# Kernel optimization log

Hardware: AMD Instinct MI355X
Metric: run time of the kernel (lower is better)

## Reference

```python
import jax, jax.numpy as jnp
import numpy as np


def _segmented_exclusive_cumsum(vals, seg_start_flags):
    """Exclusive cumsum of vals that resets at segment starts (flags True)."""
    def combine(a, b):
        va, fa = a
        vb, fb = b
        return (jnp.where(fb, vb, va + vb), fa | fb)
    inclusive, _ = jax.lax.associative_scan(combine, (vals, seg_start_flags))
    return inclusive - vals


def setup_inputs() -> dict:
    key = jax.random.key(0)
    k1, k2 = jax.random.split(key)
    n_rays = 65536
    samples_per_ray = 128  # average; ragged via sorted random ray ids
    n_pts = n_rays * samples_per_ray  # 8_388_608 sample points
    density = jax.random.normal(k1, (n_pts,), dtype=jnp.float32)
    ray_id = jnp.sort(jax.random.randint(k2, (n_pts,), 0, n_rays)).astype(jnp.int32)
    shift = jnp.float32(-3.0)      # self.act_shift
    interval = jnp.float32(0.5)    # stepsize * voxel_size_ratio
    return {"density": density, "shift": shift, "interval": interval,
            "ray_id": ray_id, "n_rays": n_rays}


def reference(density, shift, interval, ray_id, n_rays):
    # Raw2Alpha: alpha = 1 - exp(-softplus(density + shift) * interval)
    # log(1 - alpha) = -interval * softplus(density + shift)  (stable, no log of tiny)
    log_one_minus_alpha = -interval * jax.nn.softplus(density + shift)
    alpha = 1.0 - jnp.exp(log_one_minus_alpha)

    # Alphas2Weights: per-ray exclusive cumprod of (1 - alpha) in log space.
    # ray_id is sorted; segment starts where the ray id changes.
    seg_start = jnp.concatenate(
        [jnp.ones((1,), dtype=bool), ray_id[1:] != ray_id[:-1]])
    log_T = _segmented_exclusive_cumsum(log_one_minus_alpha, seg_start)
    T = jnp.exp(log_T)                      # transmittance before each sample
    weights = alpha * T                     # [n_pts]

    # alphainv_last[r] = prod over ray r of (1 - alpha) = residual transmittance
    log_total = jax.ops.segment_sum(log_one_minus_alpha, ray_id,
                                    num_segments=n_rays)
    alphainv_last = jnp.exp(log_total)      # [n_rays]; empty rays -> exp(0)=1
    return weights, alphainv_last
```

## Files before the change

### kernel.cpp

```cpp
#include <hip/hip_runtime.h>
#include <math.h>


#define LOG2E 1.4426950408889634f
#define EPT   8
#define BPTS  (256 * EPT)
#define NXCD  8

typedef float vf4 __attribute__((ext_vector_type(4)));

__device__ __forceinline__ float exp2f_(float x) { return __builtin_amdgcn_exp2f(x); }
__device__ __forceinline__ float log2f_(float x) { return __builtin_amdgcn_logf(x); }
__device__ __forceinline__ float rsqf_(float x)  { return __builtin_amdgcn_rsqf(x); }

__device__ __forceinline__ float oma(float d, float sh2, float negc, bool fast) {
    const float y = fmaf(d, LOG2E, sh2);
    if (fast) return rsqf_(1.0f + exp2f_(y));
    const float sp = fmaxf(y, 0.f) + log2f_(1.f + exp2f_(-fabsf(y)));
    return exp2f_(negc * sp);
}

template <int CTRL, int RM>
__device__ __forceinline__ void seg_step(float& V, int& F) {
    const int vs_i = __builtin_amdgcn_update_dpp(
        0x3f800000, __builtin_bit_cast(int, V), CTRL, RM, 0xF, false);
    const int fs = __builtin_amdgcn_update_dpp(0, F, CTRL, RM, 0xF, false);
    const float vs = __builtin_bit_cast(float, vs_i);
    V = F ? V : vs * V;
    F = F | fs;
}

__device__ __forceinline__ float wave_prod_bcast(float x) {
#define STEPP(CTRL, RM)                                                        \
    { int t_ = __builtin_amdgcn_update_dpp(0x3f800000,                         \
          __builtin_bit_cast(int, x), CTRL, RM, 0xF, false);                   \
      x *= __builtin_bit_cast(float, t_); }
    STEPP(0x111, 0xF) STEPP(0x112, 0xF) STEPP(0x114, 0xF)
    STEPP(0x118, 0xF) STEPP(0x142, 0xA) STEPP(0x143, 0xC)
#undef STEPP
    return __builtin_bit_cast(float,
        __builtin_amdgcn_readlane(__builtin_bit_cast(int, x), 63));
}

__device__ __forceinline__ int wave_imax_bcast(int x) {
#define STEPM(CTRL, RM)                                                        \
    { int t_ = __builtin_amdgcn_update_dpp((int)0x80000000, x, CTRL, RM,       \
                                           0xF, false);                        \
      x = (x > t_) ? x : t_; }
    STEPM(0x111, 0xF) STEPM(0x112, 0xF) STEPM(0x114, 0xF)
    STEPM(0x118, 0xF) STEPM(0x142, 0xA) STEPM(0x143, 0xC)
#undef STEPM
    return __builtin_amdgcn_readlane(x, 63);
}

__global__ void __launch_bounds__(256)
fused_alpha_weights(const float* __restrict__ density,
                    const int*   __restrict__ ray_id,
                    const float* __restrict__ shift_p,
                    const float* __restrict__ interval_p,
                    float* __restrict__ weights,
                    float* __restrict__ alphainv,
                    int n_pts, int n_rays) {
    __shared__ float s_wv[4];
    __shared__ int   s_wf[4];
    __shared__ float s_red[4];
    __shared__ int   s_redi[4];

    const int t    = threadIdx.x;
    const int lane = t & 63;
    const int wid  = t >> 6;

    const int nwg  = gridDim.x;
    const int orig = blockIdx.x;
    const int qq   = nwg / NXCD, rr = nwg % NXCD;
    const int xcd  = orig % NXCD;
    const int blk  = (xcd < rr ? xcd * (qq + 1) : rr * (qq + 1) + (xcd - rr) * qq)
                   + orig / NXCD;

    const int base = blk * BPTS;
    const int idx0 = base + t * EPT;

    const float shift = shift_p[0];
    const float c     = interval_p[0];
    const float sh2   = shift * LOG2E;
    const float negc  = -c;
    const bool  fast  = (c == 0.5f);

    int r[EPT + 1]; float d[EPT]; bool v[EPT];
    if (idx0 + EPT <= n_pts) {
        const int4   ri0 = *reinterpret_cast<const int4*>(ray_id + idx0);
        const int4   ri1 = *reinterpret_cast<const int4*>(ray_id + idx0 + 4);
        const float4 de0 = *reinterpret_cast<const float4*>(density + idx0);
        const float4 de1 = *reinterpret_cast<const float4*>(density + idx0 + 4);
        r[0] = ri0.x; r[1] = ri0.y; r[2] = ri0.z; r[3] = ri0.w;
        r[4] = ri1.x; r[5] = ri1.y; r[6] = ri1.z; r[7] = ri1.w;
        d[0] = de0.x; d[1] = de0.y; d[2] = de0.z; d[3] = de0.w;
        d[4] = de1.x; d[5] = de1.y; d[6] = de1.z; d[7] = de1.w;
        #pragma unroll
        for (int k = 0; k < EPT; ++k) v[k] = true;
    } else {
        #pragma unroll
        for (int k = 0; k < EPT; ++k) {
            const int i = idx0 + k;
            v[k] = (i < n_pts);
            r[k] = v[k] ? ray_id[i] : n_rays;
            d[k] = v[k] ? density[i] : 0.0f;
        }
    }
    r[EPT] = (idx0 + EPT < n_pts) ? ray_id[idx0 + EPT] : n_rays;
    const int rprev = (idx0 == 0) ? -1
                    : ((idx0 <= n_pts) ? ray_id[idx0 - 1] : n_rays);

    int w_id = 0; float w_den = 0.0f; int rfirst = 0;
    if (base > 0) {
        const int wi = base - 256 + t;
        w_id   = ray_id[wi];
        w_den  = density[wi];
        rfirst = ray_id[base];
    }

    float a[EPT]; int f[EPT];
    #pragma unroll
    for (int k = 0; k < EPT; ++k) {
        const float av = oma(d[k], sh2, negc, fast);
        a[k] = v[k] ? av : 1.0f;
        f[k] = (k == 0) ? (r[0] != rprev) : (r[k] != r[k - 1]);
    }

    float V = a[0];  int F = f[0];
    #pragma unroll
    for (int k = 1; k < EPT; ++k) {
        V = f[k] ? a[k] : V * a[k];
        F |= f[k];
    }

    float Vi = V;  int Fi = F;
    seg_step<0x111, 0xF>(Vi, Fi);
    seg_step<0x112, 0xF>(Vi, Fi);
    seg_step<0x114, 0xF>(Vi, Fi);
    seg_step<0x118, 0xF>(Vi, Fi);
    seg_step<0x142, 0xA>(Vi, Fi);
    seg_step<0x143, 0xC>(Vi, Fi);

    if (lane == 63) { s_wv[wid] = Vi; s_wf[wid] = Fi; }
    if (base > 0) {
        const int cand = (w_id != rfirst) ? t : -1;
        const int wm = wave_imax_bcast(cand);
        if (lane == 0) s_redi[wid] = wm;
    }
    __syncthreads();

    float carry0 = 1.0f;
    if (base > 0) {
        int m = s_redi[0];
        m = (s_redi[1] > m) ? s_redi[1] : m;
        m = (s_redi[2] > m) ? s_redi[2] : m;
        m = (s_redi[3] > m) ? s_redi[3] : m;
        float aa = oma(w_den, sh2, negc, fast);
        if (m >= 0 && t <= m) aa = 1.0f;
        const float wp = wave_prod_bcast(aa);
        if (lane == 0) s_red[wid] = wp;
        __syncthreads();
        carry0 = s_red[0] * s_red[1] * s_red[2] * s_red[3];

        if (m < 0) {
            int lo = base - 256;
            int s0 = -1;
            while (s0 < 0) {
                const int wstart = lo - 256;
                const int i = wstart + t;
                const int vv = (i >= 0) ? ray_id[i] : -1;
                const int c2 = (vv != rfirst) ? t : -1;
                const int wm2 = wave_imax_bcast(c2);
                if (lane == 0) s_redi[wid] = wm2;
                __syncthreads();
                int m2 = s_redi[0];
                m2 = (s_redi[1] > m2) ? s_redi[1] : m2;
                m2 = (s_redi[2] > m2) ? s_redi[2] : m2;
                m2 = (s_redi[3] > m2) ? s_redi[3] : m2;
                __syncthreads();
                if (m2 >= 0) s0 = wstart + m2 + 1; else lo = wstart;
            }
            for (int off = s0; off < base - 256; off += 256) {
                const int i = off + t;
                const float aa2 = (i < base - 256)
                                ? oma(density[i], sh2, negc, fast) : 1.0f;
                const float wp2 = wave_prod_bcast(aa2);
                if (lane == 0) s_red[wid] = wp2;
                __syncthreads();
                carry0 *= s_red[0] * s_red[1] * s_red[2] * s_red[3];
                __syncthreads();
            }
        }
    }

    float Vx = __shfl_up(Vi, 1, 64);
    int   Fx = __shfl_up(Fi, 1, 64);
    if (lane == 0) { Vx = 1.0f; Fx = 0; }

    float Ev = carry0;
    #pragma unroll
    for (int w2 = 0; w2 < 3; ++w2) {
        if (w2 < wid) {
            const float bv = s_wv[w2];  const int bf = s_wf[w2];
            Ev = bf ? bv : Ev * bv;
        }
    }
    Ev = Fx ? Vx : Ev * Vx;

    float T[EPT], e[EPT];
    float prev = Ev;
    #pragma unroll
    for (int k = 0; k < EPT; ++k) {
        T[k] = f[k] ? 1.0f : prev;
        e[k] = T[k] * a[k];
        prev = e[k];
    }

    if (idx0 + EPT <= n_pts) {
        vf4 w0 = { T[0] - e[0], T[1] - e[1], T[2] - e[2], T[3] - e[3] };
        vf4 w1 = { T[4] - e[4], T[5] - e[5], T[6] - e[6], T[7] - e[7] };
        __builtin_nontemporal_store(w0, reinterpret_cast<vf4*>(weights + idx0));
        __builtin_nontemporal_store(w1, reinterpret_cast<vf4*>(weights + idx0 + 4));
    } else {
        #pragma unroll
        for (int k = 0; k < EPT; ++k)
            if (v[k]) weights[idx0 + k] = T[k] - e[k];
    }

    #pragma unroll
    for (int k = 0; k < EPT; ++k) {
        if (v[k] && r[k] != r[k + 1]) {
            alphainv[r[k]] = e[k];
            for (int q = r[k] + 1; q < r[k + 1]; ++q) alphainv[q] = 1.0f;
        }
    }
    if (idx0 == 0) {
        for (int q = 0; q < r[0]; ++q) alphainv[q] = 1.0f;
    }
}

extern "C" void kernel_launch(void* const* d_in, const int* in_sizes, int n_in,
                              void* d_out, int out_size, void* d_ws, size_t ws_size,
                              hipStream_t stream) {
    const float* density  = (const float*)d_in[0];
    const float* shift    = (const float*)d_in[1];
    const float* interval = (const float*)d_in[2];
    const int*   ray_id   = (const int*)d_in[3];
    const int n_pts  = in_sizes[0];
    const int n_rays = out_size - n_pts;

    float* weights  = (float*)d_out;
    float* alphainv = (float*)d_out + n_pts;

    const int grid = (n_pts + BPTS - 1) / BPTS;
    fused_alpha_weights<<<grid, 256, 0, stream>>>(
        density, ray_id, shift, interval, weights, alphainv, n_pts, n_rays);
}
```

Before: 22.73 us.

## Use 512-thread blocks and share neighbor ray ids through LDS

Doubles the block size to 512 threads so each block covers twice as many points, which halves the number of 256-point lookback windows fetched per point. Per-thread neighbor ray ids (previous and next) now come from shared memory instead of extra scattered global loads. The lookback max-reduction is moved before the first barrier so the carry product can share the second barrier, removing one sync. The cost is more waves per block (8 instead of 4), a longer cross-wave carry chain, and possibly lower occupancy flexibility.

```diff
diff --git a/kernel.cpp b/kernel.cpp
--- a/kernel.cpp
+++ b/kernel.cpp
@@ -4,7 +4,9 @@
 
 #define LOG2E 1.4426950408889634f
 #define EPT   8
-#define BPTS  (256 * EPT)
+#define NTHR  512
+#define BPTS  (NTHR * EPT)
+#define WIN   256
 #define NXCD  8
 
 typedef float vf4 __attribute__((ext_vector_type(4)));
@@ -53,7 +55,7 @@
     return __builtin_amdgcn_readlane(x, 63);
 }
 
-__global__ void __launch_bounds__(256)
+__global__ void __launch_bounds__(NTHR)
 fused_alpha_weights(const float* __restrict__ density,
                     const int*   __restrict__ ray_id,
                     const float* __restrict__ shift_p,
@@ -61,10 +63,13 @@
                     float* __restrict__ weights,
                     float* __restrict__ alphainv,
                     int n_pts, int n_rays) {
-    __shared__ float s_wv[4];
-    __shared__ int   s_wf[4];
-    __shared__ float s_red[4];
-    __shared__ int   s_redi[4];
+    __shared__ int   s_first[NTHR];
+    __shared__ int   s_last[NTHR];
+    __shared__ float s_wv[8];
+    __shared__ int   s_wf[8];
+    __shared__ float s_red[8];
+    __shared__ int   s_redi[8];
+    __shared__ int   s_prevlast;
 
     const int t    = threadIdx.x;
     const int lane = t & 63;
@@ -107,17 +112,36 @@
             d[k] = v[k] ? density[i] : 0.0f;
         }
     }
-    r[EPT] = (idx0 + EPT < n_pts) ? ray_id[idx0 + EPT] : n_rays;
-    const int rprev = (idx0 == 0) ? -1
-                    : ((idx0 <= n_pts) ? ray_id[idx0 - 1] : n_rays);
+    int r8next = n_rays;
+    if (t == NTHR - 1 && base + BPTS < n_pts) r8next = ray_id[base + BPTS];
 
     int w_id = 0; float w_den = 0.0f; int rfirst = 0;
     if (base > 0) {
-        const int wi = base - 256 + t;
-        w_id   = ray_id[wi];
-        w_den  = density[wi];
         rfirst = ray_id[base];
-    }
+        if (t < WIN) {
+            const int wi = base - WIN + t;
+            w_id  = ray_id[wi];
+            w_den = density[wi];
+        }
+    }
+
+    s_first[t] = r[0];
+    s_last[t]  = r[EPT - 1];
+    if (base > 0 && t == WIN - 1) s_prevlast = w_id;
+    {
+        const int cand = (base > 0 && t < WIN && w_id != rfirst) ? t : -1;
+        const int wm = wave_imax_bcast(cand);
+        if (lane == 0) s_redi[wid] = wm;
+    }
+    __syncthreads();
+
+    const int rprev = (t > 0) ? s_last[t - 1]
+                    : (base == 0 ? -1 : s_prevlast);
+    r[EPT] = (t < NTHR - 1) ? s_first[t + 1] : r8next;
+
+    int m = s_redi[0];
+    #pragma unroll
+    for (int w2 = 1; w2 < 8; ++w2) m = (s_redi[w2] > m) ? s_redi[w2] : m;
 
     float a[EPT]; int f[EPT];
     #pragma unroll
@@ -142,53 +166,58 @@
     seg_step<0x142, 0xA>(Vi, Fi);
     seg_step<0x143, 0xC>(Vi, Fi);
 
+    if (base > 0) {
+        float aa = 1.0f;
+        if (t < WIN) {
+            aa = oma(w_den, sh2, negc, fast);
+            if (m >= 0 && t <= m) aa = 1.0f;
+        }
+        const float wp = wave_prod_bcast(aa);
+        if (lane == 0) s_red[wid] = wp;
+    }
     if (lane == 63) { s_wv[wid] = Vi; s_wf[wid] = Fi; }
-    if (base > 0) {
-        const int cand = (w_id != rfirst) ? t : -1;
-        const int wm = wave_imax_bcast(cand);
-        if (lane == 0) s_redi[wid] = wm;
-    }
     __syncthreads();
 
     float carry0 = 1.0f;
     if (base > 0) {
-        int m = s_redi[0];
-        m = (s_redi[1] > m) ? s_redi[1] : m;
-        m = (s_redi[2] > m) ? s_redi[2] : m;
-        m = (s_redi[3] > m) ? s_redi[3] : m;
-        float aa = oma(w_den, sh2, negc, fast);
-        if (m >= 0 && t <= m) aa = 1.0f;
-        const float wp = wave_prod_bcast(aa);
-        if (lane == 0) s_red[wid] = wp;
-        __syncthreads();
-        carry0 = s_red[0] * s_red[1] * s_red[2] * s_red[3];
+        carry0 = s_red[0];
+        #pragma unroll
+        for (int w2 = 1; w2 < 8; ++w2) carry0 *= s_red[w2];
 
         if (m < 0) {
-            int lo = base - 256;
+            int lo = base - WIN;
             int s0 = -1;
             while (s0 < 0) {
-                const int wstart = lo - 256;
-                const int i = wstart + t;
-                const int vv = (i >= 0) ? ray_id[i] : -1;
-                const int c2 = (vv != rfirst) ? t : -1;
+                const int wstart = lo - WIN;
+                int c2 = -1;
+                if (t < WIN) {
+                    const int i = wstart + t;
+                    const int vv = (i >= 0) ? ray_id[i] : -1;
+                    c2 = (vv != rfirst) ? t : -1;
+                }
                 const int wm2 = wave_imax_bcast(c2);
                 if (lane == 0) s_redi[wid] = wm2;
                 __syncthreads();
                 int m2 = s_redi[0];
-                m2 = (s_redi[1] > m2) ? s_redi[1] : m2;
-                m2 = (s_redi[2] > m2) ? s_redi[2] : m2;
-                m2 = (s_redi[3] > m2) ? s_redi[3] : m2;
+                #pragma unroll
+                for (int w2 = 1; w2 < 8; ++w2)
+                    m2 = (s_redi[w2] > m2) ? s_redi[w2] : m2;
                 __syncthreads();
                 if (m2 >= 0) s0 = wstart + m2 + 1; else lo = wstart;
             }
-            for (int off = s0; off < base - 256; off += 256) {
-                const int i = off + t;
-                const float aa2 = (i < base - 256)
-                                ? oma(density[i], sh2, negc, fast) : 1.0f;
+            for (int off = s0; off < base - WIN; off += WIN) {
+                float aa2 = 1.0f;
+                if (t < WIN) {
+                    const int i = off + t;
+                    if (i < base - WIN) aa2 = oma(density[i], sh2, negc, fast);
+                }
                 const float wp2 = wave_prod_bcast(aa2);
                 if (lane == 0) s_red[wid] = wp2;
                 __syncthreads();
-                carry0 *= s_red[0] * s_red[1] * s_red[2] * s_red[3];
+                float pp = s_red[0];
+                #pragma unroll
+                for (int w2 = 1; w2 < 8; ++w2) pp *= s_red[w2];
+                carry0 *= pp;
                 __syncthreads();
             }
         }
@@ -200,7 +229,7 @@
 
     float Ev = carry0;
     #pragma unroll
-    for (int w2 = 0; w2 < 3; ++w2) {
+    for (int w2 = 0; w2 < 7; ++w2) {
         if (w2 < wid) {
             const float bv = s_wv[w2];  const int bf = s_wf[w2];
             Ev = bf ? bv : Ev * bv;
@@ -254,6 +283,6 @@
     float* alphainv = (float*)d_out + n_pts;
 
     const int grid = (n_pts + BPTS - 1) / BPTS;
-    fused_alpha_weights<<<grid, 256, 0, stream>>>(
+    fused_alpha_weights<<<grid, NTHR, 0, stream>>>(
         density, ray_id, shift, interval, weights, alphainv, n_pts, n_rays);
 }
```

Result: slower. 24.10 us (+6.0%).
